# Performance work log

Hardware: AMD Instinct MI355X
Metric: run time of the kernel (lower is better)

## Reference

```python
import jax, jax.numpy as jnp
import numpy as np
from jax import lax

EPS = 1e-5
K = 32  # k_neighbor

def conv1(x, w):
    # x: [B, Cin, L], w: [Cout, Cin] (1x1 conv, no bias)
    return jnp.einsum('bcl,oc->bol', x, w)

def bn(x, g, b):
    # BatchNorm1d in training mode: batch statistics over (batch, length)
    m = jnp.mean(x, axis=(0, 2), keepdims=True)
    v = jnp.var(x, axis=(0, 2), keepdims=True)
    return g[None, :, None] * (x - m) / jnp.sqrt(v + EPS) + b[None, :, None]

def res_block(x, w1, g1, b1, w2, g2, b2):
    h = jax.nn.gelu(bn(conv1(x, w1), g1, b1), approximate=False)
    h = bn(conv1(h, w2), g2, b2)
    return jax.nn.gelu(h + x, approximate=False)

def extraction(x, conv_w, bn_g, bn_b, fw, fg, fb):
    # conv_w: [n_blocks, 2, C, C]; bn_g/bn_b: [n_blocks, 2, C]
    for i in range(conv_w.shape[0]):
        x = res_block(x, conv_w[i, 0], bn_g[i, 0], bn_b[i, 0],
                      conv_w[i, 1], bn_g[i, 1], bn_b[i, 1])
    # TransformerBlock: ffn (conv+BN) with residual + GELU
    return jax.nn.gelu(x + bn(conv1(x, fw), fg, fb), approximate=False)

def setup_inputs() -> dict:
    key = jax.random.key(0)
    ks = jax.random.split(key, 16)
    B, N, S, C = 8, 4096, 1024, 128  # C = out_channel = 2*channel
    inp = {
        'xyz': jax.random.normal(ks[0], (B, N, 3), dtype=jnp.float32),
        'x': jax.random.normal(ks[1], (B, 64, N), dtype=jnp.float32),
        'fps_idx': jax.random.randint(ks[2], (B, S), 0, N, dtype=jnp.int64),
        'pre_conv_w': jax.random.normal(ks[3], (2, 2, C, C), dtype=jnp.float32) * 0.05,
        'pre_bn_g': jnp.ones((2, 2, C), jnp.float32),
        'pre_bn_b': jnp.zeros((2, 2, C), jnp.float32),
        'pre_ffn_w': jax.random.normal(ks[4], (C, C), dtype=jnp.float32) * 0.05,
        'pre_ffn_g': jnp.ones((C,), jnp.float32),
        'pre_ffn_b': jnp.zeros((C,), jnp.float32),
        'pos_conv_w': jax.random.normal(ks[5], (2, 2, C, C), dtype=jnp.float32) * 0.05,
        'pos_bn_g': jnp.ones((2, 2, C), jnp.float32),
        'pos_bn_b': jnp.zeros((2, 2, C), jnp.float32),
        'pos_ffn_w': jax.random.normal(ks[6], (C, C), dtype=jnp.float32) * 0.05,
        'pos_ffn_g': jnp.ones((C,), jnp.float32),
        'pos_ffn_b': jnp.zeros((C,), jnp.float32),
    }
    return inp

def reference(xyz, x, fps_idx,
              pre_conv_w, pre_bn_g, pre_bn_b, pre_ffn_w, pre_ffn_g, pre_ffn_b,
              pos_conv_w, pos_bn_g, pos_bn_b, pos_ffn_w, pos_ffn_g, pos_ffn_b):
    B, N, _ = xyz.shape
    S = fps_idx.shape[1]
    points = jnp.swapaxes(x, 1, 2)  # [B, N, d]
    d = points.shape[-1]

    # --- LocalGrouper ---
    new_xyz = jnp.take_along_axis(xyz, fps_idx[:, :, None], axis=1)      # [B, S, 3]
    new_pts = jnp.take_along_axis(points, fps_idx[:, :, None], axis=1)  # [B, S, d]

    # squared distances [B, S, N]
    sqr = (jnp.sum(new_xyz ** 2, -1)[:, :, None]
           + jnp.sum(xyz ** 2, -1)[:, None, :]
           - 2.0 * jnp.einsum('bsc,bnc->bsn', new_xyz, xyz))
    idx = lax.top_k(-sqr, K)[1]  # [B, S, K] smallest distances

    grouped = jnp.take_along_axis(points, idx.reshape(B, S * K)[:, :, None],
                                  axis=1).reshape(B, S, K, d)
    center = new_pts[:, :, None, :]  # [B, S, 1, d]
    feat = jnp.concatenate([grouped - center,
                            jnp.broadcast_to(center, grouped.shape)], axis=-1)  # [B,S,K,2d]

    C = 2 * d
    # --- PreExtraction: [B,S,K,C] -> [B*S, C, K] -> maxpool -> [B, C, S] ---
    y = jnp.swapaxes(feat, 2, 3).reshape(B * S, C, K)
    y = extraction(y, pre_conv_w, pre_bn_g, pre_bn_b, pre_ffn_w, pre_ffn_g, pre_ffn_b)
    y = jnp.max(y, axis=-1).reshape(B, S, C)
    y = jnp.swapaxes(y, 1, 2)  # [B, C, S]

    # --- PosExtraction ---
    y = extraction(y, pos_conv_w, pos_bn_g, pos_bn_b, pos_ffn_w, pos_ffn_g, pos_ffn_b)
    return (new_xyz, y)
```

## Files before the change

kernel.cpp:

```cpp
#include <hip/hip_runtime.h>
#include <math.h>

typedef unsigned short ushort_t;
typedef unsigned long long u64;
typedef unsigned int uint32;

#define B_ 8
#define N_ 4096
#define S_ 1024
#define K_ 32
#define C_ 128
#define NCOL1 (B_*S_*K_)
#define NCOL2 (B_*S_)
#define EPS_ 1e-5f

typedef ushort_t us8 __attribute__((ext_vector_type(8)));
typedef short s16x8 __attribute__((ext_vector_type(8)));
typedef float f32x4 __attribute__((ext_vector_type(4)));

__device__ __forceinline__ float bf2f(ushort_t u){ return __uint_as_float(((uint32)u)<<16); }
__device__ __forceinline__ ushort_t f2bf(float f){
    uint32 x = __float_as_uint(f);
    return (ushort_t)((x + 0x7FFFu + ((x>>16)&1u)) >> 16);
}
__device__ __forceinline__ float gelu_f(float v){
    float az = fabsf(v)*0.70710678118654752f;
    float t  = __builtin_amdgcn_rcpf(fmaf(0.3275911f, az, 1.0f));
    float p  = fmaf(fmaf(fmaf(fmaf(1.061405429f, t, -1.453152027f), t, 1.421413741f), t,
                   -0.284496736f), t, 0.254829592f)*t;
    float e  = __expf(-az*az);
    float er = fmaf(-p, e, 1.0f);
    float s  = (v < 0.0f) ? -er : er;
    return 0.5f*v*(1.0f+s);
}
__device__ __forceinline__ u64 shfl_xor_u64(u64 v, int m){
    int lo = __shfl_xor((int)(v & 0xFFFFFFFFull), m, 64);
    int hi = __shfl_xor((int)(v >> 32), m, 64);
    return (((u64)(uint32)hi) << 32) | (uint32)lo;
}
__device__ __forceinline__ void gl_lds16(const char* gp, char* lp){
    __builtin_amdgcn_global_load_lds((const __attribute__((address_space(1))) void*)gp,
                                     (__attribute__((address_space(3))) void*)lp, 16, 0, 0);
}

__global__ __launch_bounds__(256) void transpose_kernel(const float* __restrict__ x, ushort_t* __restrict__ xTb){
    __shared__ float t[64][65];
    int b  = blockIdx.x >> 6;
    int n0 = (blockIdx.x & 63) * 64;
    int tx = threadIdx.x & 63, ty = threadIdx.x >> 6;
    #pragma unroll
    for (int i=0;i<16;i++){
        int c = i*4 + ty;
        t[c][tx] = x[((long)(b*64 + c))*N_ + n0 + tx];
    }
    __syncthreads();
    #pragma unroll
    for (int i=0;i<16;i++){
        int n = i*4 + ty;
        xTb[((long)(b*N_ + n0 + n))*64 + tx] = f2bf(t[tx][n]);
    }
}

__global__ __launch_bounds__(256) void knn_kernel(const float* __restrict__ xyz, const int* __restrict__ fps,
                                                  int* __restrict__ idxg, float* __restrict__ newxyz){
    __shared__ uint32 hist[4096];
    __shared__ u64    cand[1024];
    __shared__ u64    out_keys[64];
    __shared__ uint32 csum[256];
    __shared__ uint32 wtot[4];
    __shared__ uint32 shv[8];
    __shared__ u64    wred[4];
    __shared__ u64    winner;

    int tid = threadIdx.x;
    int wv = tid >> 6, l = tid & 63;
    int bs = blockIdx.x;
    int b  = bs >> 10;
    int qi = fps[bs];
    const float* qb = xyz + ((long)b*N_ + qi)*3;
    float qx = qb[0], qy = qb[1], qz = qb[2];
    if (tid < 3) newxyz[(long)bs*3 + tid] = qb[tid];
    const float* xb = xyz + (long)b*N_*3;

    for (int i=tid;i<1024;i+=256) hist[i]=0;
    if (tid < 8) shv[tid]=0;
    __syncthreads();

    uint32 dbits[16];
    #pragma unroll
    for (int i=0;i<16;i++){
        int n = i*256 + tid;
        float dx = xb[n*3+0]-qx, dy = xb[n*3+1]-qy, dz = xb[n*3+2]-qz;
        float d = dx*dx + dy*dy + dz*dz;
        dbits[i] = __float_as_uint(d);
        atomicAdd(&hist[dbits[i]>>21], 1u);
    }
    __syncthreads();

    {
        uint32 h4[4]; uint32 csumv=0;
        #pragma unroll
        for (int i=0;i<4;i++){ h4[i]=hist[tid*4+i]; csumv+=h4[i]; }
        uint32 sc = csumv;
        #pragma unroll
        for (int off=1; off<64; off<<=1){ uint32 o=__shfl_up(sc,off,64); if (l>=off) sc+=o; }
        if (l==63) wtot[wv]=sc;
        csum[tid]=sc;
        __syncthreads();
        uint32 base=0;
        for (int w2=0; w2<wv; w2++) base += wtot[w2];
        uint32 cum = base + csum[tid] - csumv;
        #pragma unroll
        for (int i=0;i<4;i++){
            if (cum <= 31u && 31u < cum + h4[i]){ shv[0]=(uint32)(tid*4+i); shv[1]=cum; }
            cum += h4[i];
        }
    }
    __syncthreads();
    uint32 b1 = shv[0], cl1 = shv[1];

    for (int i=tid;i<4096;i+=256) hist[i]=0;
    __syncthreads();
    #pragma unroll
    for (int i=0;i<16;i++){
        uint32 u = dbits[i];
        if ((u>>21)==b1) atomicAdd(&hist[(u>>9)&0xFFFu], 1u);
    }
    __syncthreads();

    uint32 r2 = 31u - cl1;
    {
        uint32 h[16]; uint32 csumv=0;
        #pragma unroll
        for (int i=0;i<16;i++){ h[i]=hist[tid*16+i]; csumv += h[i]; }
        uint32 sc = csumv;
        #pragma unroll
        for (int off=1; off<64; off<<=1){ uint32 o=__shfl_up(sc,off,64); if (l>=off) sc+=o; }
        if (l==63) wtot[wv]=sc;
        csum[tid]=sc;
        __syncthreads();
        uint32 base=0;
        for (int w2=0; w2<wv; w2++) base += wtot[w2];
        uint32 cum = base + csum[tid] - csumv;
        #pragma unroll
        for (int i=0;i<16;i++){
            if (cum <= r2 && r2 < cum + h[i]){ shv[2]=(uint32)(tid*16+i); shv[3]=cum; }
            cum += h[i];
        }
    }
    __syncthreads();
    uint32 b2 = shv[2], cl2 = shv[3];
    uint32 nless = cl1 + cl2;

    #pragma unroll
    for (int i=0;i<16;i++){
        uint32 u = dbits[i];
        int n = i*256 + tid;
        uint32 bb1 = u >> 21;
        if (bb1 > b1) continue;
        u64 key = (((u64)u)<<32) | (uint32)n;
        if (bb1 < b1){
            uint32 p = atomicAdd(&shv[4],1u); out_keys[p] = key;
        } else {
            uint32 bb2 = (u>>9)&0xFFFu;
            if (bb2 < b2){ uint32 p = atomicAdd(&shv[4],1u); out_keys[p] = key; }
            else if (bb2 == b2){ uint32 p = atomicAdd(&shv[5],1u); if (p < 1024u) cand[p] = key; }
        }
    }
    __syncthreads();

    if (shv[5] > 1024u){
        uint32 alive = 0xFFFFu;
        for (int r=0;r<K_;r++){
            u64 lmin = ~0ull;
            #pragma unroll
            for (int i=0;i<16;i++){
                u64 k = (((u64)dbits[i])<<32) | (uint32)(i*256+tid);
                if (((alive>>i)&1u) && k < lmin) lmin = k;
            }
            #pragma unroll
            for (int off=32; off>=1; off>>=1){
                u64 o = shfl_xor_u64(lmin, off);
                if (o < lmin) lmin = o;
            }
            if (l == 0) wred[wv] = lmin;
            __syncthreads();
            if (tid == 0){
                u64 m = wred[0];
                if (wred[1]<m) m=wred[1];
                if (wred[2]<m) m=wred[2];
                if (wred[3]<m) m=wred[3];
                winner = m;
                idxg[(long)bs*K_ + r] = (int)(m & 0xFFFFFFFFull);
            }
            __syncthreads();
            u64 w = winner;
            #pragma unroll
            for (int i=0;i<16;i++){
                u64 k = (((u64)dbits[i])<<32) | (uint32)(i*256+tid);
                if (k == w) alive &= ~(1u<<i);
            }
        }
    } else if (wv == 0){
        uint32 cb   = shv[5];
        uint32 need = 32u - nless;
        for (uint32 r=0; r<need; r++){
            u64 lmin = ~0ull;
            for (uint32 s=l; s<cb; s+=64){ u64 kk = cand[s]; if (kk < lmin) lmin = kk; }
            #pragma unroll
            for (int off=32; off>=1; off>>=1){
                u64 o = shfl_xor_u64(lmin, off);
                if (o < lmin) lmin = o;
            }
            for (uint32 s=l; s<cb; s+=64){ if (cand[s]==lmin) cand[s] = ~0ull; }
            if (l==0) out_keys[nless + r] = lmin;
        }
        u64 key = (l < 32) ? out_keys[l] : ~0ull;
        #pragma unroll
        for (uint32 k=2; k<=64; k<<=1){
            bool dir = ((l & k)==0);
            #pragma unroll
            for (uint32 j=k>>1; j>=1; j>>=1){
                u64 o = shfl_xor_u64(key, j);
                bool lower = ((l & j)==0);
                u64 mn = (key < o) ? key : o;
                u64 mx = (key < o) ? o : key;
                key = (lower == dir) ? mn : mx;
            }
        }
        if (l < 32) idxg[(long)bs*K_ + l] = (int)(key & 0xFFFFFFFFull);
    }
}

__global__ __launch_bounds__(256) void wcvt_kernel(const float* __restrict__ pcw, const float* __restrict__ pfw,
                                                   const float* __restrict__ qcw, const float* __restrict__ qfw,
                                                   ushort_t* __restrict__ Wb, ushort_t* __restrict__ UW,
                                                   ushort_t* __restrict__ VW){
    int i = blockIdx.x*256 + threadIdx.x;
    if (i < 163840){
        int mat = i >> 14;
        int r = i & 16383;
        float v;
        if (mat < 4)       v = pcw[i];
        else if (mat == 4) v = pfw[r];
        else if (mat < 9)  v = qcw[i - 5*16384];
        else               v = qfw[r];
        Wb[i] = f2bf(v);
    } else {
        int j = i - 163840;
        int jj = j & 8191;
        int oc = jj >> 6, c = jj & 63;
        if (j < 8192) UW[jj] = f2bf(pcw[oc*128 + c]);
        else          VW[jj] = f2bf(pcw[oc*128 + 64 + c] - pcw[oc*128 + c]);
    }
}

__global__ __launch_bounds__(256) void uv_gemm(const ushort_t* __restrict__ xTb, const int* __restrict__ fps,
                                               const ushort_t* __restrict__ UW, const ushort_t* __restrict__ VW,
                                               ushort_t* __restrict__ U, ushort_t* __restrict__ V2){
    int tid = threadIdx.x;
    int w = tid >> 6, l = tid & 63;
    int l15 = l & 15, l4 = l >> 4;
    bool isV = blockIdx.x >= 256;
    int base = (isV ? (int)(blockIdx.x - 256) : (int)blockIdx.x)*128 + w*32;
    const ushort_t* Wh = isV ? VW : UW;
    ushort_t* out = isV ? V2 : U;

    long xrow[2];
    #pragma unroll
    for (int n=0;n<2;n++){
        int r = base + n*16 + l15;
        if (isV){ int b = r >> 10; xrow[n] = ((long)(b<<12) + fps[r]); }
        else    { xrow[n] = r; }
    }
    f32x4 acc[8][2] = {};
    #pragma unroll
    for (int ks=0; ks<2; ks++){
        int kl = ks*32 + l4*8;
        s16x8 af[8];
        #pragma unroll
        for (int m=0;m<8;m++)
            af[m] = *(const s16x8*)(Wh + (m*16 + l15)*64 + kl);
        s16x8 bv[2];
        #pragma unroll
        for (int n=0;n<2;n++)
            bv[n] = *(const s16x8*)(xTb + xrow[n]*64 + kl);
        #pragma unroll
        for (int m=0;m<8;m++)
            #pragma unroll
            for (int n=0;n<2;n++)
                acc[m][n] = __builtin_amdgcn_mfma_f32_16x16x32_bf16(af[m], bv[n], acc[m][n], 0, 0, 0);
    }
    #pragma unroll
    for (int n=0;n<2;n++){
        long radr = (long)(base + n*16 + l15)*C_;
        #pragma unroll
        for (int m=0;m<8;m++){
            f32x4 a = acc[m][n];
            uint2 st;
            st.x = (((uint32)f2bf(a[1]))<<16) | f2bf(a[0]);
            st.y = (((uint32)f2bf(a[3]))<<16) | f2bf(a[2]);
            *(uint2*)(out + radr + m*16 + l4*4) = st;
        }
    }
}

template<int MODE>
__global__ __launch_bounds__(256) void conv_mfma(const ushort_t* in1, const ushort_t* in2, ushort_t* aux,
                                                 ushort_t* out, const ushort_t* __restrict__ Wb,
                                                 const float* __restrict__ scsh_g,
                                                 const ushort_t* __restrict__ U, const ushort_t* __restrict__ V2,
                                                 const ushort_t* __restrict__ xTb, const int* __restrict__ idxg,
                                                 const int* __restrict__ fps,
                                                 float* __restrict__ pb, int nb, float inv_cnt){
    __shared__ ushort_t inT[16384];
    __shared__ float ss[256];
    __shared__ float sL[4][128], qL[4][128];
    int tid = threadIdx.x;
    int w = tid >> 6, l = tid & 63;
    int l15 = l & 15, l4 = l >> 4;
    long col0 = ((long)blockIdx.x << 7) + ((long)w << 5);

    if (MODE != 3){
        const char* gt = (const char*)(in1 + (((long)blockIdx.x) << 7)*C_);
        char* lb = (char*)inT;
        #pragma unroll
        for (int i=0;i<8;i++){
            int p = i*4096 + w*1024 + l*16;
            int src = p ^ (((p>>8)&7)<<4);
            gl_lds16(gt + src, lb + i*4096 + w*1024);
        }
    }

    s16x8 a2[8];
    if (MODE == 2){
        #pragma unroll
        for (int t=0;t<8;t++){
            int n = t>>2, ks = t&3;
            a2[t] = *(const s16x8*)(in2 + (col0 + n*16 + l15)*C_ + ks*32 + l4*8);
        }
    }
    if (MODE == 4){
        int bs = (int)(col0 >> 5);
        int b  = bs >> 10;
        int cc = fps[bs];
        const ushort_t* crow = xTb + ((long)(b<<12) + cc)*64;
        s16x8 c0 = *(const s16x8*)(crow + l4*8);
        s16x8 c1 = *(const s16x8*)(crow + 32 + l4*8);
        #pragma unroll
        for (int n=0;n<2;n++){
            int nn = idxg[col0 + n*16 + l15];
            const ushort_t* prow = xTb + ((long)(b<<12) + nn)*64;
            s16x8 p0 = *(const s16x8*)(prow + l4*8);
            s16x8 p1 = *(const s16x8*)(prow + 32 + l4*8);
            s16x8 d0, d1;
            #pragma unroll
            for (int e=0;e<8;e++){
                d0[e] = (short)f2bf(bf2f((ushort_t)p0[e]) - bf2f((ushort_t)c0[e]));
                d1[e] = (short)f2bf(bf2f((ushort_t)p1[e]) - bf2f((ushort_t)c1[e]));
            }
            a2[n*4+0] = d0; a2[n*4+1] = d1; a2[n*4+2] = c0; a2[n*4+3] = c1;
        }
    }
    if (MODE == 1 || MODE == 2 || MODE == 4) ss[tid] = scsh_g[tid];
    __syncthreads();

    f32x4 acc[8][2] = {};
    if (MODE == 3){
        int bs = (int)(col0 >> 5);
        int b  = bs >> 10;
        const ushort_t* vrow = V2 + (long)bs*C_;
        #pragma unroll
        for (int n=0;n<2;n++){
            int nn = idxg[col0 + n*16 + l15];
            const ushort_t* urow = U + ((long)(b*4096) + nn)*C_;
            #pragma unroll
            for (int m=0;m<8;m++){
                int oc0 = m*16 + l4*4;
                uint2 uu = *(const uint2*)(urow + oc0);
                uint2 vv = *(const uint2*)(vrow + oc0);
                acc[m][n][0] = bf2f((ushort_t)(uu.x & 0xFFFFu)) + bf2f((ushort_t)(vv.x & 0xFFFFu));
                acc[m][n][1] = bf2f((ushort_t)(uu.x >> 16))     + bf2f((ushort_t)(vv.x >> 16));
                acc[m][n][2] = bf2f((ushort_t)(uu.y & 0xFFFFu)) + bf2f((ushort_t)(vv.y & 0xFFFFu));
                acc[m][n][3] = bf2f((ushort_t)(uu.y >> 16))     + bf2f((ushort_t)(vv.y >> 16));
            }
        }
    } else {
        char* lb = (char*)inT;
        #pragma unroll
        for (int ks=0; ks<4; ks++){
            int kl = ks*32 + l4*8;
            s16x8 af[8];
            #pragma unroll
            for (int m=0;m<8;m++)
                af[m] = *(const s16x8*)(Wb + (m*16 + l15)*C_ + kl);
            s16x8 bv[2];
            int qsv[2];
            #pragma unroll
            for (int n=0;n<2;n++){
                int q = (w*32 + n*16 + l15)*256 + ks*64 + l4*16;
                qsv[n] = q ^ (((q>>8)&7)<<4);
                bv[n] = *(const s16x8*)(lb + qsv[n]);
            }
            {
                float sc[8], sh[8];
                const float4* sp = (const float4*)(&ss[kl*2]);
                float4 s0 = sp[0], s1 = sp[1], s2 = sp[2], s3 = sp[3];
                sc[0]=s0.x; sh[0]=s0.y; sc[1]=s0.z; sh[1]=s0.w;
                sc[2]=s1.x; sh[2]=s1.y; sc[3]=s1.z; sh[3]=s1.w;
                sc[4]=s2.x; sh[4]=s2.y; sc[5]=s2.z; sh[5]=s2.w;
                sc[6]=s3.x; sh[6]=s3.y; sc[7]=s3.z; sh[7]=s3.w;
                #pragma unroll
                for (int n=0;n<2;n++){
                    s16x8 v = bv[n];
                    if (MODE == 1){
                        #pragma unroll
                        for (int e=0;e<8;e++){
                            float f = gelu_f(fmaf(bf2f((ushort_t)v[e]), sc[e], sh[e]));
                            v[e] = (short)f2bf(f);
                        }
                    } else {
                        s16x8 a = a2[n*4+ks];
                        #pragma unroll
                        for (int e=0;e<8;e++){
                            float f = gelu_f(fmaf(bf2f((ushort_t)v[e]), sc[e], sh[e]) + bf2f((ushort_t)a[e]));
                            v[e] = (short)f2bf(f);
                        }
                    }
                    bv[n] = v;
                    if (MODE == 2 || MODE == 4)
                        *(s16x8*)(lb + qsv[n]) = v;
                }
            }
            #pragma unroll
            for (int m=0;m<8;m++)
                #pragma unroll
                for (int n=0;n<2;n++)
                    acc[m][n] = __builtin_amdgcn_mfma_f32_16x16x32_bf16(af[m], bv[n], acc[m][n], 0, 0, 0);
        }
    }

    if (MODE == 2 || MODE == 4){
        __syncthreads();
        char* auxb = (char*)aux + ((long)blockIdx.x << 15);
        const char* lb = (const char*)inT;
        #pragma unroll
        for (int i=0;i<8;i++){
            int lin = i*4096 + tid*16;
            int qs = lin ^ (((lin>>8)&7)<<4);
            *(f32x4*)(auxb + lin) = *(const f32x4*)(lb + qs);
        }
        __syncthreads();
    }

    {
        char* lb = (char*)inT;
        #pragma unroll
        for (int n=0;n<2;n++){
            #pragma unroll
            for (int m=0;m<8;m++){
                f32x4 a = acc[m][n];
                uint2 st;
                st.x = (((uint32)f2bf(a[1]))<<16) | f2bf(a[0]);
                st.y = (((uint32)f2bf(a[3]))<<16) | f2bf(a[2]);
                int q = (w*32 + n*16 + l15)*256 + (m*16 + l4*4)*2;
                int qs = q ^ (((q>>8)&7)<<4);
                *(uint2*)(lb + qs) = st;
            }
        }
        __syncthreads();
        char* outb = (char*)out + ((long)blockIdx.x << 15);
        const char* lb2 = (const char*)inT;
        #pragma unroll
        for (int i=0;i<8;i++){
            int lin = i*4096 + tid*16;
            int qs = lin ^ (((lin>>8)&7)<<4);
            *(f32x4*)(outb + lin) = *(const f32x4*)(lb2 + qs);
        }
    }

    #pragma unroll
    for (int m=0;m<8;m++){
        #pragma unroll
        for (int r=0;r<4;r++){
            float a0=acc[m][0][r], a1=acc[m][1][r];
            float s = a0+a1;
            float q = a0*a0+a1*a1;
            #pragma unroll
            for (int off=1; off<16; off<<=1){
                s += __shfl_xor(s, off, 64);
                q += __shfl_xor(q, off, 64);
            }
            if (l15 == 0){
                sL[w][m*16 + l4*4 + r] = s;
                qL[w][m*16 + l4*4 + r] = q;
            }
        }
    }
    __syncthreads();
    if (tid < 128){
        float s = sL[0][tid] + sL[1][tid] + sL[2][tid] + sL[3][tid];
        float q = qL[0][tid] + qL[1][tid] + qL[2][tid] + qL[3][tid];
        pb[(long)tid*nb + blockIdx.x]       = s;
        pb[(long)(128+tid)*nb + blockIdx.x] = q;
    }
}

__global__ __launch_bounds__(256) void reduce_fin_kernel(const float* __restrict__ pb, float* __restrict__ scsh,
                                                         const float* __restrict__ g, const float* __restrict__ bb,
                                                         float inv_cnt, int nb){
    int oc = blockIdx.x;
    float s=0.f, q=0.f;
    for (int b=threadIdx.x; b<nb; b+=256){
        s += pb[(long)oc*nb + b];
        q += pb[(long)(128+oc)*nb + b];
    }
    __shared__ float ls[256], lq[256];
    ls[threadIdx.x]=s; lq[threadIdx.x]=q;
    __syncthreads();
    #pragma unroll
    for (int st_=128; st_>0; st_>>=1){
        if (threadIdx.x < st_){ ls[threadIdx.x]+=ls[threadIdx.x+st_]; lq[threadIdx.x]+=lq[threadIdx.x+st_]; }
        __syncthreads();
    }
    if (threadIdx.x==0){
        float mean = ls[0]*inv_cnt;
        float var  = lq[0]*inv_cnt - mean*mean;
        float sc   = g[oc]*rsqrtf(var + EPS_);
        scsh[oc*2+0] = sc;
        scsh[oc*2+1] = bb[oc] - mean*sc;
    }
}

__global__ __launch_bounds__(256) void pool_kernel(const ushort_t* __restrict__ T, const ushort_t* __restrict__ X,
                                                   const float* __restrict__ scsh, ushort_t* __restrict__ A2){
    long p  = (long)blockIdx.x*256 + threadIdx.x;
    long bs = p >> 6;
    int  c0 = ((int)p & 63)*2;
    float sc0=scsh[c0*2], sh0=scsh[c0*2+1], sc1=scsh[c0*2+2], sh1=scsh[c0*2+3];
    const ushort_t* tb = T + (bs*K_)*(long)C_ + c0;
    const ushort_t* xv = X + (bs*K_)*(long)C_ + c0;
    float m0 = -1e30f, m1 = -1e30f;
    #pragma unroll 4
    for (int k=0;k<K_;k++){
        uint32 tv = *(const uint32*)(tb + (long)k*C_);
        uint32 av = *(const uint32*)(xv + (long)k*C_);
        float v0 = gelu_f(fmaf(bf2f((ushort_t)(tv & 0xFFFFu)), sc0, sh0) + bf2f((ushort_t)(av & 0xFFFFu)));
        float v1 = gelu_f(fmaf(bf2f((ushort_t)(tv >> 16)),     sc1, sh1) + bf2f((ushort_t)(av >> 16)));
        m0 = fmaxf(m0, v0);
        m1 = fmaxf(m1, v1);
    }
    uint32 o = (((uint32)f2bf(m1))<<16) | f2bf(m0);
    *(uint32*)(A2 + bs*C_ + c0) = o;
}

__device__ __forceinline__ void gbar(uint32* cnt, uint32 target){
    __threadfence();
    __syncthreads();
    if (threadIdx.x == 0){
        __hip_atomic_fetch_add(cnt, 1u, __ATOMIC_RELEASE, __HIP_MEMORY_SCOPE_AGENT);
        while (__hip_atomic_load(cnt, __ATOMIC_ACQUIRE, __HIP_MEMORY_SCOPE_AGENT) < target){
            __builtin_amdgcn_s_sleep(4);
        }
        __threadfence();
    }
    __syncthreads();
    __threadfence();
}

template<int M>
__device__ __forceinline__ void e2_phase(ushort_t* Ts, ushort_t* Xs, const ushort_t* Wp,
                                         const float* ss, int w, int l15, int l4,
                                         f32x4 (&acc)[8][2]){
    char* tb = (char*)Ts;
    char* xb = (char*)Xs;
    const char* src = (M==0) ? (const char*)xb : (const char*)tb;
    #pragma unroll
    for (int ks=0; ks<4; ks++){
        int kl = ks*32 + l4*8;
        s16x8 af[8];
        #pragma unroll
        for (int m=0;m<8;m++)
            af[m] = *(const s16x8*)(Wp + (m*16 + l15)*C_ + kl);
        #pragma unroll
        for (int n=0;n<2;n++){
            int q  = (w*32 + n*16 + l15)*256 + ks*64 + l4*16;
            int qs = q ^ (((q>>8)&7)<<4);
            s16x8 v = *(const s16x8*)(src + qs);
            if (M >= 1){
                const float4* sp = (const float4*)(&ss[kl*2]);
                float4 s0=sp[0], s1=sp[1], s2=sp[2], s3=sp[3];
                float sc[8] = {s0.x,s0.z,s1.x,s1.z,s2.x,s2.z,s3.x,s3.z};
                float sh[8] = {s0.y,s0.w,s1.y,s1.w,s2.y,s2.w,s3.y,s3.w};
                s16x8 xv;
                if (M == 2) xv = *(const s16x8*)(xb + qs);
                #pragma unroll
                for (int e=0;e<8;e++){
                    float f = fmaf(bf2f((ushort_t)v[e]), sc[e], sh[e]);
                    if (M == 2) f += bf2f((ushort_t)xv[e]);
                    f = gelu_f(f);
                    v[e] = (short)f2bf(f);
                }
                if (M == 2) *(s16x8*)(xb + qs) = v;
            }
            #pragma unroll
            for (int m=0;m<8;m++)
                acc[m][n] = __builtin_amdgcn_mfma_f32_16x16x32_bf16(af[m], v, acc[m][n], 0, 0, 0);
        }
    }
    asm volatile("s_waitcnt lgkmcnt(0)" ::: "memory");
    __builtin_amdgcn_sched_barrier(0);
    #pragma unroll
    for (int n=0;n<2;n++){
        #pragma unroll
        for (int m=0;m<8;m++){
            f32x4 a = acc[m][n];
            uint2 st;
            st.x = (((uint32)f2bf(a[1]))<<16) | f2bf(a[0]);
            st.y = (((uint32)f2bf(a[3]))<<16) | f2bf(a[2]);
            int q2  = (w*32 + n*16 + l15)*256 + (m*16 + l4*4)*2;
            int qs2 = q2 ^ (((q2>>8)&7)<<4);
            *(uint2*)(tb + qs2) = st;
        }
    }
}

__global__ __launch_bounds__(256) void ext2_kernel(const ushort_t* __restrict__ A2, const ushort_t* __restrict__ Wq,
        const float* __restrict__ bng, const float* __restrict__ bnb,
        const float* __restrict__ fg, const float* __restrict__ fb,
        float* __restrict__ pbE, uint32* cnt, float* __restrict__ y, float inv_cnt){
    __shared__ ushort_t Ts[16384];
    __shared__ ushort_t Xs[16384];
    __shared__ float ss[256];
    __shared__ float sL[4][128], qL[4][128];
    int tid = threadIdx.x, w = tid>>6, l = tid&63, l15 = l&15, l4 = l>>4;
    int blk = blockIdx.x;

    {
        const char* gt = (const char*)(A2 + ((long)blk << 7)*C_);
        #pragma unroll
        for (int i=0;i<8;i++){
            int p = i*4096 + w*1024 + l*16;
            int src = p ^ (((p>>8)&7)<<4);
            gl_lds16(gt + src, (char*)Xs + i*4096 + w*1024);
        }
    }
    __syncthreads();

    #pragma unroll
    for (int ph=0; ph<5; ph++){
        f32x4 acc[8][2] = {};
        if      (ph==0) e2_phase<0>(Ts, Xs, Wq + 0*C_*C_, ss, w, l15, l4, acc);
        else if (ph==1) e2_phase<1>(Ts, Xs, Wq + 1*C_*C_, ss, w, l15, l4, acc);
        else if (ph==2) e2_phase<2>(Ts, Xs, Wq + 2*C_*C_, ss, w, l15, l4, acc);
        else if (ph==3) e2_phase<1>(Ts, Xs, Wq + 3*C_*C_, ss, w, l15, l4, acc);
        else            e2_phase<2>(Ts, Xs, Wq + 4*C_*C_, ss, w, l15, l4, acc);

        #pragma unroll
        for (int m=0;m<8;m++){
            #pragma unroll
            for (int r=0;r<4;r++){
                float a0=acc[m][0][r], a1=acc[m][1][r];
                float s=a0+a1, q=a0*a0+a1*a1;
                #pragma unroll
                for (int off=1; off<16; off<<=1){
                    s += __shfl_xor(s, off, 64);
                    q += __shfl_xor(q, off, 64);
                }
                if (l15 == 0){ sL[w][m*16+l4*4+r]=s; qL[w][m*16+l4*4+r]=q; }
            }
        }
        __syncthreads();
        float* pbS = pbE + ph*16384;
        if (tid < 128){
            float s = sL[0][tid]+sL[1][tid]+sL[2][tid]+sL[3][tid];
            float q = qL[0][tid]+qL[1][tid]+qL[2][tid]+qL[3][tid];
            pbS[tid*64 + blk]       = s;
            pbS[(128+tid)*64 + blk] = q;
        }
        gbar(cnt, 64u*(uint32)(ph+1));
        if (tid < 128){
            float s=0.f, q=0.f;
            #pragma unroll 8
            for (int k=0;k<64;k++){ s += pbS[tid*64+k]; q += pbS[(128+tid)*64+k]; }
            float mean = s*inv_cnt, var = q*inv_cnt - mean*mean;
            float gg = (ph<4) ? bng[ph*128 + tid] : fg[tid];
            float bv = (ph<4) ? bnb[ph*128 + tid] : fb[tid];
            float sc = gg*rsqrtf(var + EPS_);
            ss[tid*2]   = sc;
            ss[tid*2+1] = bv - mean*sc;
        }
        __syncthreads();
    }

    int b  = blk >> 3;
    int s0 = (blk & 7) * 128;
    int colL = tid & 127;
    int rep  = tid >> 7;
    #pragma unroll
    for (int cb=0; cb<8; cb++){
        int q  = colL*256 + rep*128 + cb*16;
        int qs = q ^ (((q>>8)&7)<<4);
        s16x8 tvv = *(const s16x8*)((char*)Ts + qs);
        s16x8 xvv = *(const s16x8*)((char*)Xs + qs);
        #pragma unroll
        for (int e=0;e<8;e++){
            int c = rep*64 + cb*8 + e;
            float f = gelu_f(fmaf(bf2f((ushort_t)tvv[e]), ss[c*2], ss[c*2+1]) + bf2f((ushort_t)xvv[e]));
            y[((long)(b*C_ + c))*S_ + s0 + colL] = f;
        }
    }
}

extern "C" void kernel_launch(void* const* d_in, const int* in_sizes, int n_in,
                              void* d_out, int out_size, void* d_ws, size_t ws_size,
                              hipStream_t stream){
    const float* xyz        = (const float*)d_in[0];
    const float* x          = (const float*)d_in[1];
    const int*   fps        = (const int*)d_in[2];
    const float* pre_conv_w = (const float*)d_in[3];
    const float* pre_bn_g   = (const float*)d_in[4];
    const float* pre_bn_b   = (const float*)d_in[5];
    const float* pre_ffn_w  = (const float*)d_in[6];
    const float* pre_ffn_g  = (const float*)d_in[7];
    const float* pre_ffn_b  = (const float*)d_in[8];
    const float* pos_conv_w = (const float*)d_in[9];
    const float* pos_bn_g   = (const float*)d_in[10];
    const float* pos_bn_b   = (const float*)d_in[11];
    const float* pos_ffn_w  = (const float*)d_in[12];
    const float* pos_ffn_g  = (const float*)d_in[13];
    const float* pos_ffn_b  = (const float*)d_in[14];

    float* out_xyz = (float*)d_out;
    float* out_y   = (float*)d_out + (long)B_*S_*3;

    char* ws = (char*)d_ws;
    float*    scsh = (float*)(ws + 0);
    uint32*   cnt  = (uint32*)(ws + 8192);
    float*    pbE  = (float*)(ws + 10240);
    ushort_t* Wb   = (ushort_t*)(ws + 337920);
    ushort_t* UW   = (ushort_t*)(ws + 665600);
    ushort_t* VW   = (ushort_t*)(ws + 681984);
    int*      idx  = (int*)(ws + 698368);
    ushort_t* xTb  = (ushort_t*)(ws + 1746944);
    ushort_t* A2   = (ushort_t*)(ws + 5941248);
    float*    pb1  = (float*)(ws + 8038400);
    ushort_t* Cb   = (ushort_t*)(ws + 10135552);
    ushort_t* X    = (ushort_t*)(ws + 77244416);
    ushort_t* U    = (ushort_t*)(ws + 77244416);
    ushort_t* V2   = (ushort_t*)(ws + 85633024);
    (void)in_sizes; (void)n_in; (void)out_size; (void)ws_size;

    const float inv1 = 1.0f/(float)NCOL1, inv2 = 1.0f/(float)NCOL2;
    const ushort_t* Wp = Wb;
    const ushort_t* Wq = Wb + 5*C_*C_;
    const int nb = 2048;

    hipMemsetAsync(cnt, 0, 64, stream);
    wcvt_kernel<<<704,256,0,stream>>>(pre_conv_w, pre_ffn_w, pos_conv_w, pos_ffn_w, Wb, UW, VW);
    transpose_kernel<<<B_*(N_/64),256,0,stream>>>(x, xTb);
    knn_kernel<<<B_*S_,256,0,stream>>>(xyz, fps, idx, out_xyz);
    uv_gemm<<<320,256,0,stream>>>(xTb, fps, UW, VW, U, V2);

    {
        const float* G[5]  = {pre_bn_g, pre_bn_g+C_, pre_bn_g+2*C_, pre_bn_g+3*C_, pre_ffn_g};
        const float* Bv[5] = {pre_bn_b, pre_bn_b+C_, pre_bn_b+2*C_, pre_bn_b+3*C_, pre_ffn_b};
        conv_mfma<3><<<nb,256,0,stream>>>(nullptr, nullptr, nullptr, Cb, nullptr, nullptr,
                                          U, V2, nullptr, idx, fps, pb1, nb, inv1);
        reduce_fin_kernel<<<128,256,0,stream>>>(pb1, scsh+0*256, G[0], Bv[0], inv1, nb);
        conv_mfma<1><<<nb,256,0,stream>>>(Cb, nullptr, nullptr, Cb, Wp+1*C_*C_, scsh+0*256,
                                          nullptr, nullptr, nullptr, nullptr, nullptr, pb1, nb, inv1);
        reduce_fin_kernel<<<128,256,0,stream>>>(pb1, scsh+1*256, G[1], Bv[1], inv1, nb);
        conv_mfma<4><<<nb,256,0,stream>>>(Cb, nullptr, X, Cb, Wp+2*C_*C_, scsh+1*256,
                                          nullptr, nullptr, xTb, idx, fps, pb1, nb, inv1);
        reduce_fin_kernel<<<128,256,0,stream>>>(pb1, scsh+2*256, G[2], Bv[2], inv1, nb);
        conv_mfma<1><<<nb,256,0,stream>>>(Cb, nullptr, nullptr, Cb, Wp+3*C_*C_, scsh+2*256,
                                          nullptr, nullptr, nullptr, nullptr, nullptr, pb1, nb, inv1);
        reduce_fin_kernel<<<128,256,0,stream>>>(pb1, scsh+3*256, G[3], Bv[3], inv1, nb);
        conv_mfma<2><<<nb,256,0,stream>>>(Cb, X, X, Cb, Wp+4*C_*C_, scsh+3*256,
                                          nullptr, nullptr, nullptr, nullptr, nullptr, pb1, nb, inv1);
        reduce_fin_kernel<<<128,256,0,stream>>>(pb1, scsh+4*256, G[4], Bv[4], inv1, nb);
        pool_kernel<<<(NCOL2*64)/256,256,0,stream>>>(Cb, X, scsh+4*256, A2);
    }

    ext2_kernel<<<64,256,0,stream>>>(A2, Wq, pos_bn_g, pos_bn_b, pos_ffn_g, pos_ffn_b,
                                     pbE, cnt, out_y, inv2);
}
```

Measured before the change: 649.2 us.

## Replace persistent grid-barrier PosExtraction kernel with per-layer conv and reduce launches

Measured after the change: 583.5 us. -10.1%, faster.

```diff
diff --git a/kernel.cpp b/kernel.cpp
--- a/kernel.cpp
+++ b/kernel.cpp
@@ -402,7 +402,7 @@
                 qsv[n] = q ^ (((q>>8)&7)<<4);
                 bv[n] = *(const s16x8*)(lb + qsv[n]);
             }
-            {
+            if (MODE != 0){
                 float sc[8], sh[8];
                 const float4* sp = (const float4*)(&ss[kl*2]);
                 float4 s0 = sp[0], s1 = sp[1], s2 = sp[2], s3 = sp[3];
@@ -554,144 +554,27 @@
     *(uint32*)(A2 + bs*C_ + c0) = o;
 }
 
-__device__ __forceinline__ void gbar(uint32* cnt, uint32 target){
-    __threadfence();
-    __syncthreads();
-    if (threadIdx.x == 0){
-        __hip_atomic_fetch_add(cnt, 1u, __ATOMIC_RELEASE, __HIP_MEMORY_SCOPE_AGENT);
-        while (__hip_atomic_load(cnt, __ATOMIC_ACQUIRE, __HIP_MEMORY_SCOPE_AGENT) < target){
-            __builtin_amdgcn_s_sleep(4);
-        }
-        __threadfence();
-    }
-    __syncthreads();
-    __threadfence();
-}
-
-template<int M>
-__device__ __forceinline__ void e2_phase(ushort_t* Ts, ushort_t* Xs, const ushort_t* Wp,
-                                         const float* ss, int w, int l15, int l4,
-                                         f32x4 (&acc)[8][2]){
-    char* tb = (char*)Ts;
-    char* xb = (char*)Xs;
-    const char* src = (M==0) ? (const char*)xb : (const char*)tb;
-    #pragma unroll
-    for (int ks=0; ks<4; ks++){
-        int kl = ks*32 + l4*8;
-        s16x8 af[8];
-        #pragma unroll
-        for (int m=0;m<8;m++)
-            af[m] = *(const s16x8*)(Wp + (m*16 + l15)*C_ + kl);
-        #pragma unroll
-        for (int n=0;n<2;n++){
-            int q  = (w*32 + n*16 + l15)*256 + ks*64 + l4*16;
-            int qs = q ^ (((q>>8)&7)<<4);
-            s16x8 v = *(const s16x8*)(src + qs);
-            if (M >= 1){
-                const float4* sp = (const float4*)(&ss[kl*2]);
-                float4 s0=sp[0], s1=sp[1], s2=sp[2], s3=sp[3];
-                float sc[8] = {s0.x,s0.z,s1.x,s1.z,s2.x,s2.z,s3.x,s3.z};
-                float sh[8] = {s0.y,s0.w,s1.y,s1.w,s2.y,s2.w,s3.y,s3.w};
-                s16x8 xv;
-                if (M == 2) xv = *(const s16x8*)(xb + qs);
-                #pragma unroll
-                for (int e=0;e<8;e++){
-                    float f = fmaf(bf2f((ushort_t)v[e]), sc[e], sh[e]);
-                    if (M == 2) f += bf2f((ushort_t)xv[e]);
-                    f = gelu_f(f);
-                    v[e] = (short)f2bf(f);
-                }
-                if (M == 2) *(s16x8*)(xb + qs) = v;
-            }
-            #pragma unroll
-            for (int m=0;m<8;m++)
-                acc[m][n] = __builtin_amdgcn_mfma_f32_16x16x32_bf16(af[m], v, acc[m][n], 0, 0, 0);
-        }
-    }
-    asm volatile("s_waitcnt lgkmcnt(0)" ::: "memory");
-    __builtin_amdgcn_sched_barrier(0);
-    #pragma unroll
-    for (int n=0;n<2;n++){
-        #pragma unroll
-        for (int m=0;m<8;m++){
-            f32x4 a = acc[m][n];
-            uint2 st;
-            st.x = (((uint32)f2bf(a[1]))<<16) | f2bf(a[0]);
-            st.y = (((uint32)f2bf(a[3]))<<16) | f2bf(a[2]);
-            int q2  = (w*32 + n*16 + l15)*256 + (m*16 + l4*4)*2;
-            int qs2 = q2 ^ (((q2>>8)&7)<<4);
-            *(uint2*)(tb + qs2) = st;
-        }
-    }
-}
-
-__global__ __launch_bounds__(256) void ext2_kernel(const ushort_t* __restrict__ A2, const ushort_t* __restrict__ Wq,
-        const float* __restrict__ bng, const float* __restrict__ bnb,
-        const float* __restrict__ fg, const float* __restrict__ fb,
-        float* __restrict__ pbE, uint32* cnt, float* __restrict__ y, float inv_cnt){
+__global__ __launch_bounds__(256) void out2_kernel(const ushort_t* __restrict__ T, const ushort_t* __restrict__ X,
+                                                   const float* __restrict__ scsh_g, float* __restrict__ y){
     __shared__ ushort_t Ts[16384];
     __shared__ ushort_t Xs[16384];
     __shared__ float ss[256];
-    __shared__ float sL[4][128], qL[4][128];
-    int tid = threadIdx.x, w = tid>>6, l = tid&63, l15 = l&15, l4 = l>>4;
+    int tid = threadIdx.x, w = tid>>6, l = tid&63;
     int blk = blockIdx.x;
 
     {
-        const char* gt = (const char*)(A2 + ((long)blk << 7)*C_);
+        const char* gt = (const char*)(T + ((long)blk << 7)*C_);
+        const char* gx = (const char*)(X + ((long)blk << 7)*C_);
         #pragma unroll
         for (int i=0;i<8;i++){
             int p = i*4096 + w*1024 + l*16;
             int src = p ^ (((p>>8)&7)<<4);
-            gl_lds16(gt + src, (char*)Xs + i*4096 + w*1024);
-        }
-    }
-    __syncthreads();
-
-    #pragma unroll
-    for (int ph=0; ph<5; ph++){
-        f32x4 acc[8][2] = {};
-        if      (ph==0) e2_phase<0>(Ts, Xs, Wq + 0*C_*C_, ss, w, l15, l4, acc);
-        else if (ph==1) e2_phase<1>(Ts, Xs, Wq + 1*C_*C_, ss, w, l15, l4, acc);
-        else if (ph==2) e2_phase<2>(Ts, Xs, Wq + 2*C_*C_, ss, w, l15, l4, acc);
-        else if (ph==3) e2_phase<1>(Ts, Xs, Wq + 3*C_*C_, ss, w, l15, l4, acc);
-        else            e2_phase<2>(Ts, Xs, Wq + 4*C_*C_, ss, w, l15, l4, acc);
-
-        #pragma unroll
-        for (int m=0;m<8;m++){
-            #pragma unroll
-            for (int r=0;r<4;r++){
-                float a0=acc[m][0][r], a1=acc[m][1][r];
-                float s=a0+a1, q=a0*a0+a1*a1;
-                #pragma unroll
-                for (int off=1; off<16; off<<=1){
-                    s += __shfl_xor(s, off, 64);
-                    q += __shfl_xor(q, off, 64);
-                }
-                if (l15 == 0){ sL[w][m*16+l4*4+r]=s; qL[w][m*16+l4*4+r]=q; }
-            }
-        }
-        __syncthreads();
-        float* pbS = pbE + ph*16384;
-        if (tid < 128){
-            float s = sL[0][tid]+sL[1][tid]+sL[2][tid]+sL[3][tid];
-            float q = qL[0][tid]+qL[1][tid]+qL[2][tid]+qL[3][tid];
-            pbS[tid*64 + blk]       = s;
-            pbS[(128+tid)*64 + blk] = q;
-        }
-        gbar(cnt, 64u*(uint32)(ph+1));
-        if (tid < 128){
-            float s=0.f, q=0.f;
-            #pragma unroll 8
-            for (int k=0;k<64;k++){ s += pbS[tid*64+k]; q += pbS[(128+tid)*64+k]; }
-            float mean = s*inv_cnt, var = q*inv_cnt - mean*mean;
-            float gg = (ph<4) ? bng[ph*128 + tid] : fg[tid];
-            float bv = (ph<4) ? bnb[ph*128 + tid] : fb[tid];
-            float sc = gg*rsqrtf(var + EPS_);
-            ss[tid*2]   = sc;
-            ss[tid*2+1] = bv - mean*sc;
-        }
-        __syncthreads();
-    }
+            gl_lds16(gt + src, (char*)Ts + i*4096 + w*1024);
+            gl_lds16(gx + src, (char*)Xs + i*4096 + w*1024);
+        }
+    }
+    ss[tid] = scsh_g[tid];
+    __syncthreads();
 
     int b  = blk >> 3;
     int s0 = (blk & 7) * 128;
@@ -736,7 +619,6 @@
 
     char* ws = (char*)d_ws;
     float*    scsh = (float*)(ws + 0);
-    uint32*   cnt  = (uint32*)(ws + 8192);
     float*    pbE  = (float*)(ws + 10240);
     ushort_t* Wb   = (ushort_t*)(ws + 337920);
     ushort_t* UW   = (ushort_t*)(ws + 665600);
@@ -745,6 +627,7 @@
     ushort_t* xTb  = (ushort_t*)(ws + 1746944);
     ushort_t* A2   = (ushort_t*)(ws + 5941248);
     float*    pb1  = (float*)(ws + 8038400);
+    ushort_t* C2   = (ushort_t*)(ws + 8038400);
     ushort_t* Cb   = (ushort_t*)(ws + 10135552);
     ushort_t* X    = (ushort_t*)(ws + 77244416);
     ushort_t* U    = (ushort_t*)(ws + 77244416);
@@ -756,7 +639,6 @@
     const ushort_t* Wq = Wb + 5*C_*C_;
     const int nb = 2048;
 
-    hipMemsetAsync(cnt, 0, 64, stream);
     wcvt_kernel<<<704,256,0,stream>>>(pre_conv_w, pre_ffn_w, pos_conv_w, pos_ffn_w, Wb, UW, VW);
     transpose_kernel<<<B_*(N_/64),256,0,stream>>>(x, xTb);
     knn_kernel<<<B_*S_,256,0,stream>>>(xyz, fps, idx, out_xyz);
@@ -783,6 +665,25 @@
         pool_kernel<<<(NCOL2*64)/256,256,0,stream>>>(Cb, X, scsh+4*256, A2);
     }
 
-    ext2_kernel<<<64,256,0,stream>>>(A2, Wq, pos_bn_g, pos_bn_b, pos_ffn_g, pos_ffn_b,
-                                     pbE, cnt, out_y, inv2);
-}
+    {
+        const float* G[5]  = {pos_bn_g, pos_bn_g+C_, pos_bn_g+2*C_, pos_bn_g+3*C_, pos_ffn_g};
+        const float* Bv[5] = {pos_bn_b, pos_bn_b+C_, pos_bn_b+2*C_, pos_bn_b+3*C_, pos_ffn_b};
+        const int nb2 = 64;
+        conv_mfma<0><<<nb2,256,0,stream>>>(A2, nullptr, nullptr, C2, Wq+0*C_*C_, nullptr,
+                                           nullptr, nullptr, nullptr, nullptr, nullptr, pbE, nb2, inv2);
+        reduce_fin_kernel<<<128,256,0,stream>>>(pbE, scsh+5*256, G[0], Bv[0], inv2, nb2);
+        conv_mfma<1><<<nb2,256,0,stream>>>(C2, nullptr, nullptr, C2, Wq+1*C_*C_, scsh+5*256,
+                                           nullptr, nullptr, nullptr, nullptr, nullptr, pbE, nb2, inv2);
+        reduce_fin_kernel<<<128,256,0,stream>>>(pbE, scsh+6*256, G[1], Bv[1], inv2, nb2);
+        conv_mfma<2><<<nb2,256,0,stream>>>(C2, A2, A2, C2, Wq+2*C_*C_, scsh+6*256,
+                                           nullptr, nullptr, nullptr, nullptr, nullptr, pbE, nb2, inv2);
+        reduce_fin_kernel<<<128,256,0,stream>>>(pbE, scsh+7*256, G[2], Bv[2], inv2, nb2);
+        conv_mfma<1><<<nb2,256,0,stream>>>(C2, nullptr, nullptr, C2, Wq+3*C_*C_, scsh+7*256,
+                                           nullptr, nullptr, nullptr, nullptr, nullptr, pbE, nb2, inv2);
+        reduce_fin_kernel<<<128,256,0,stream>>>(pbE, scsh+8*256, G[3], Bv[3], inv2, nb2);
+        conv_mfma<2><<<nb2,256,0,stream>>>(C2, A2, A2, C2, Wq+4*C_*C_, scsh+8*256,
+                                           nullptr, nullptr, nullptr, nullptr, nullptr, pbE, nb2, inv2);
+        reduce_fin_kernel<<<128,256,0,stream>>>(pbE, scsh+9*256, G[4], Bv[4], inv2, nb2);
+        out2_kernel<<<64,256,0,stream>>>(C2, A2, scsh+9*256, out_y);
+    }
+}
```
